# Kernel optimization log

Hardware: AMD Instinct MI355X
Metric: run time of the kernel (lower is better)

The kernel has to match this reference:

```python
import jax, jax.numpy as jnp
import numpy as np

NUM_CLUSTERS = 16
HIDDEN = 1024
BOTTLENECK = 128
N_TOKENS = 65536


def setup_inputs() -> dict:
    key = jax.random.key(0)
    k_h, k_ids, k_w1, k_b1, k_w2, k_b2 = jax.random.split(key, 6)
    h = jax.random.normal(k_h, (N_TOKENS, HIDDEN), dtype=jnp.float32)
    cluster_ids = jax.random.randint(k_ids, (N_TOKENS,), 0, NUM_CLUSTERS)
    # Stacked per-cluster adapter params (torch Linear: y = x @ W.T + b; we store
    # already-transposed weights so forward is x @ W1[c]).
    s1 = 1.0 / np.sqrt(HIDDEN)
    s2 = 1.0 / np.sqrt(BOTTLENECK)
    W1 = jax.random.uniform(k_w1, (NUM_CLUSTERS, HIDDEN, BOTTLENECK), jnp.float32, -s1, s1)
    b1 = jax.random.uniform(k_b1, (NUM_CLUSTERS, BOTTLENECK), jnp.float32, -s1, s1)
    # Original inits these to zero; use small random values so grads are non-trivial.
    W2 = jax.random.uniform(k_w2, (NUM_CLUSTERS, BOTTLENECK, HIDDEN), jnp.float32, -s2, s2) * 0.02
    b2 = jax.random.uniform(k_b2, (NUM_CLUSTERS, HIDDEN), jnp.float32, -s2, s2) * 0.02
    return {"h": h, "cluster_ids": cluster_ids, "W1": W1, "b1": b1, "W2": W2, "b2": b2}


def reference(h, cluster_ids, W1, b1, W2, b2):
    # h: [N, H]; cluster_ids: [N]; W1: [K, H, B]; b1: [K, B]; W2: [K, B, H]; b2: [K, H]
    # out[n] = h[n] + adapter_{cluster_ids[n]}(h[n])
    K = W1.shape[0]
    out = jnp.zeros_like(h)
    for c in range(K):  # fixed small expert count; select per-token result via where
        mid = jax.nn.gelu(h @ W1[c] + b1[c], approximate=False)  # [N, B]
        y = h + mid @ W2[c] + b2[c]                               # [N, H]
        out = jnp.where((cluster_ids == c)[:, None], y, out)
    return out
```

## Files before the change

kernel.cpp:

```cpp
#include <hip/hip_runtime.h>
#include <hip/hip_bf16.h>
#include <math.h>

#define NUM_CLUSTERS 16
#define HIDDEN 1024
#define BOT 128
#define NTOK 65536

typedef __attribute__((ext_vector_type(8))) short bf16x8;
typedef __attribute__((ext_vector_type(4))) float f32x4;

typedef __attribute__((address_space(3))) unsigned int lds_u32;
typedef const __attribute__((address_space(1))) unsigned int glb_u32;

__device__ __forceinline__ void gload16(const void* g, void* l) {
  __builtin_amdgcn_global_load_lds((glb_u32*)g, (lds_u32*)l, 16, 0, 0);
}

__device__ __forceinline__ unsigned short f2bf(float x) {
  union { float f; unsigned u; } v; v.f = x;
  unsigned r = v.u + 0x7fffu + ((v.u >> 16) & 1u);
  return (unsigned short)(r >> 16);
}

__device__ __forceinline__ bf16x8 pack8(float4 a, float4 b) {
  bf16x8 r;
  r[0] = (short)f2bf(a.x); r[1] = (short)f2bf(a.y);
  r[2] = (short)f2bf(a.z); r[3] = (short)f2bf(a.w);
  r[4] = (short)f2bf(b.x); r[5] = (short)f2bf(b.y);
  r[6] = (short)f2bf(b.z); r[7] = (short)f2bf(b.w);
  return r;
}

#define SWZS(row, sidx) ((sidx) ^ (((row) & 7) << 3))
#define SW4(row, fidx) ((fidx) ^ (((row) & 7) << 2))

__device__ __forceinline__ int xcd_swz(int bid, int nwg) {
  const int nx = 8;
  int q = nwg / nx, r = nwg % nx;
  int xcd = bid % nx, idx = bid / nx;
  int b = (xcd < r) ? xcd * (q + 1) : r * (q + 1) + (xcd - r) * q;
  return b + idx;
}


__global__ void k_zero(int* p) {
  if (threadIdx.x < 64) p[threadIdx.x] = 0;
}

__global__ void k_hist(const int* __restrict__ ids, int* __restrict__ counts) {
  __shared__ int lh[NUM_CLUSTERS];
  if (threadIdx.x < NUM_CLUSTERS) lh[threadIdx.x] = 0;
  __syncthreads();
  int i = blockIdx.x * blockDim.x + threadIdx.x;
  int stride = gridDim.x * blockDim.x;
  for (; i < NTOK; i += stride) atomicAdd(&lh[ids[i]], 1);
  __syncthreads();
  if (threadIdx.x < NUM_CLUSTERS) atomicAdd(&counts[threadIdx.x], lh[threadIdx.x]);
}

__global__ void k_scan(const int* __restrict__ counts, int* __restrict__ offsets,
                       int* __restrict__ cursor) {
  if (threadIdx.x == 0 && blockIdx.x == 0) {
    int s = 0;
    for (int c = 0; c < NUM_CLUSTERS; ++c) {
      offsets[c] = s; cursor[c] = s; s += counts[c];
    }
    offsets[NUM_CLUSTERS] = s;
  }
}

__global__ void k_scatter(const int* __restrict__ ids, int* cursor,
                          int* __restrict__ perm) {
  __shared__ int lh[NUM_CLUSTERS], lbase[NUM_CLUSTERS];
  const int tid = threadIdx.x;
  if (tid < NUM_CLUSTERS) lh[tid] = 0;
  __syncthreads();
  const int i = blockIdx.x * 256 + tid;
  const int cc = ids[i];
  const int r = atomicAdd(&lh[cc], 1);
  __syncthreads();
  if (tid < NUM_CLUSTERS) lbase[tid] = atomicAdd(&cursor[tid], lh[tid]);
  __syncthreads();
  perm[lbase[cc] + r] = i;
}

__global__ void k_w1til(const float* __restrict__ W1, unsigned short* __restrict__ outw) {
  const int id = blockIdx.x * 256 + threadIdx.x;
  const int c  = id >> 14;
  const int ks = (id >> 10) & 15;
  const int q  = id & 1023;
  const int o  = q << 4;
  const int row = o >> 7;
  const int lb  = (o & 127) ^ ((row & 7) << 4);
  const int k0  = ks * 64 + (lb >> 1);
  const float* src = W1 + ((size_t)c * HIDDEN + k0) * BOT + row;
  unsigned short v[8];
  #pragma unroll
  for (int j = 0; j < 8; ++j) v[j] = f2bf(src[(size_t)j * BOT]);
  *(uint4*)((char*)outw + ((size_t)(c * 16 + ks)) * 16384 + o) = *(const uint4*)v;
}

__global__ void k_w2til(const float* __restrict__ W2, unsigned short* __restrict__ outw) {
  const int id = blockIdx.x * 256 + threadIdx.x;
  const int c  = id >> 14;
  const int nc = (id >> 10) & 15;
  const int q  = id & 1023;
  const int o  = q << 4;
  const int row = o >> 8;
  const int lb  = (o & 255) ^ ((row & 7) << 4);
  const int b0  = lb >> 1;
  const int n   = nc * 64 + row;
  const float* src = W2 + ((size_t)c * BOT + b0) * HIDDEN + n;
  unsigned short v[8];
  #pragma unroll
  for (int j = 0; j < 8; ++j) v[j] = f2bf(src[(size_t)j * HIDDEN]);
  *(uint4*)((char*)outw + ((size_t)(c * 16 + nc)) * 16384 + o) = *(const uint4*)v;
}

__device__ __forceinline__ bool locate(const int* offsets, int bid, int TMv,
                                       int& c, int& base, int& nvalid) {
  int t = bid;
  for (c = 0; c < NUM_CLUSTERS; ++c) {
    int cnt = offsets[c + 1] - offsets[c];
    int nt = (cnt + TMv - 1) / TMv;
    if (t < nt) {
      base = offsets[c] + t * TMv;
      nvalid = min(TMv, offsets[c + 1] - base);
      return true;
    }
    t -= nt;
  }
  return false;
}

#define SA1 72

__global__ __launch_bounds__(256, 3) void k_gemm1(
    const float* __restrict__ h, const float* __restrict__ b1g,
    const unsigned short* __restrict__ W1til, const int* __restrict__ offsets,
    const int* __restrict__ perm, unsigned short* __restrict__ midg) {

  __shared__ __align__(16) unsigned short sA[2][64 * SA1];
  __shared__ __align__(16) unsigned short sB[2][8192];
  __shared__ int sTok[64];

  const int tid = threadIdx.x;
  const int l = tid & 63, w = tid >> 6;
  const int lr = l & 15, lg = l >> 4;
  const int wr = w >> 1, wc = w & 1;

  const int nwg = NTOK / 64 + NUM_CLUSTERS;
  int c, base, nvalid;
  if (!locate(offsets, xcd_swz(blockIdx.x, nwg), 64, c, base, nvalid)) return;

  if (tid < 64) sTok[tid] = perm[base + min(tid, nvalid - 1)];
  __syncthreads();

  const unsigned short* w1base = W1til + (size_t)c * 16 * 8192;
  const int row = tid >> 2, q4 = tid & 3;
  const float* hrow = h + (long)sTok[row] * HIDDEN + q4 * 16;

  float4 va[4];
  #pragma unroll
  for (int j = 0; j < 4; ++j) va[j] = *(const float4*)(hrow + j * 4);
  #pragma unroll
  for (int j = 0; j < 4; ++j)
    gload16(w1base + j * 2048 + tid * 8, &sB[0][j * 2048 + tid * 8]);
  *(bf16x8*)&sA[0][row * SA1 + q4 * 16]     = pack8(va[0], va[1]);
  *(bf16x8*)&sA[0][row * SA1 + q4 * 16 + 8] = pack8(va[2], va[3]);
  __syncthreads();

  f32x4 acc[2][4];
  #pragma unroll
  for (int i = 0; i < 2; ++i)
    #pragma unroll
    for (int j = 0; j < 4; ++j) { f32x4 z = {0.f, 0.f, 0.f, 0.f}; acc[i][j] = z; }

  for (int t = 0; t < 16; ++t) {
    const int cur = t & 1;
    if (t < 15) {
      #pragma unroll
      for (int j = 0; j < 4; ++j) va[j] = *(const float4*)(hrow + (t + 1) * 64 + j * 4);
      #pragma unroll
      for (int j = 0; j < 4; ++j)
        gload16(w1base + (t + 1) * 8192 + j * 2048 + tid * 8,
                &sB[cur ^ 1][j * 2048 + tid * 8]);
    }
    #pragma unroll
    for (int kk = 0; kk < 2; ++kk) {
      bf16x8 af[2], bfr[4];
      #pragma unroll
      for (int mf = 0; mf < 2; ++mf) {
        const int m = wr * 32 + mf * 16 + lr;
        af[mf] = *(const bf16x8*)&sA[cur][m * SA1 + kk * 32 + lg * 8];
      }
      #pragma unroll
      for (int nf = 0; nf < 4; ++nf) {
        const int rn = wc * 64 + nf * 16 + lr;
        bfr[nf] = *(const bf16x8*)&sB[cur][SWZS(rn, rn * 64 + kk * 32 + lg * 8)];
      }
      #pragma unroll
      for (int mf = 0; mf < 2; ++mf)
        #pragma unroll
        for (int nf = 0; nf < 4; ++nf)
          acc[mf][nf] = __builtin_amdgcn_mfma_f32_16x16x32_bf16(af[mf], bfr[nf], acc[mf][nf], 0, 0, 0);
    }
    if (t < 15) {
      *(bf16x8*)&sA[cur ^ 1][row * SA1 + q4 * 16]     = pack8(va[0], va[1]);
      *(bf16x8*)&sA[cur ^ 1][row * SA1 + q4 * 16 + 8] = pack8(va[2], va[3]);
    }
    __syncthreads();
  }

  float b1v[4];
  #pragma unroll
  for (int nf = 0; nf < 4; ++nf) b1v[nf] = b1g[c * BOT + wc * 64 + nf * 16 + lr];
  #pragma unroll
  for (int mf = 0; mf < 2; ++mf) {
    #pragma unroll
    for (int nf = 0; nf < 4; ++nf) {
      #pragma unroll
      for (int r = 0; r < 4; ++r) {
        float x = acc[mf][nf][r] + b1v[nf];
        float g = 0.5f * x * (1.0f + erff(x * 0.70710678118654752f));
        const int m = wr * 32 + mf * 16 + lg * 4 + r;
        if (m < nvalid) {
          const int n = wc * 64 + nf * 16 + lr;
          midg[(size_t)(base + m) * BOT + n] = f2bf(g);
        }
      }
    }
  }
}


__global__ __launch_bounds__(512, 6) void k_gemm2(
    const float* __restrict__ h, const float* __restrict__ b2g,
    const unsigned short* __restrict__ W2til, const int* __restrict__ offsets,
    const int* __restrict__ perm, const unsigned short* __restrict__ midg,
    float* __restrict__ out) {

  __shared__ __align__(16) unsigned short sM[8192];
  __shared__ __align__(16) unsigned short sB[2][8192];
  __shared__ int sTok[64];

  const int tid = threadIdx.x;
  const int l = tid & 63, w = tid >> 6;
  const int lr = l & 15, lg = l >> 4;
  const int wr = w >> 2, wc = w & 3;

  const int nwg = NTOK / 64 + NUM_CLUSTERS;
  int c, base, nvalid;
  if (!locate(offsets, xcd_swz(blockIdx.x, nwg), 64, c, base, nvalid)) return;

  if (tid < 64) sTok[tid] = perm[base + min(tid, nvalid - 1)];

  const unsigned short* w2base = W2til + (size_t)c * 16 * 8192;

  gload16(w2base + tid * 8, &sB[0][tid * 8]);
  gload16(w2base + 4096 + tid * 8, &sB[0][4096 + tid * 8]);
  {
    const int row = tid >> 3, oct = tid & 7;
    const int srow = base + min(row, nvalid - 1);
    const uint4* ms = (const uint4*)(midg + (size_t)srow * BOT + oct * 16);
    uint4 m0 = ms[0], m1 = ms[1];
    *(uint4*)&sM[SWZS(row, row * 128 + oct * 16)]     = m0;
    *(uint4*)&sM[SWZS(row, row * 128 + oct * 16 + 8)] = m1;
  }
  __syncthreads();

  const int erow = tid >> 3, eo = tid & 7;
  const long etok = (long)sTok[erow] * HIDDEN;
  const float* hrow = h + etok;
  float* orow = out + etok;
  const bool evalid = erow < nvalid;

  for (int nc = 0; nc < 16; ++nc) {
    const int cur = nc & 1;
    if (nc < 15) {
      const unsigned short* w2s = w2base + (nc + 1) * 8192;
      gload16(w2s + tid * 8, &sB[cur ^ 1][tid * 8]);
      gload16(w2s + 4096 + tid * 8, &sB[cur ^ 1][4096 + tid * 8]);
    }
    float4 hv0 = *(const float4*)(hrow + nc * 64 + eo * 8);
    float4 hv1 = *(const float4*)(hrow + nc * 64 + eo * 8 + 4);
    float4 bv0 = *(const float4*)(b2g + c * HIDDEN + nc * 64 + eo * 8);
    float4 bv1 = *(const float4*)(b2g + c * HIDDEN + nc * 64 + eo * 8 + 4);

    f32x4 acc[2];
    { f32x4 z = {0.f, 0.f, 0.f, 0.f}; acc[0] = z; acc[1] = z; }
    #pragma unroll
    for (int kk = 0; kk < 4; ++kk) {
      bf16x8 af[2], bf1;
      #pragma unroll
      for (int mf = 0; mf < 2; ++mf) {
        const int m = wr * 32 + mf * 16 + lr;
        af[mf] = *(const bf16x8*)&sM[SWZS(m, m * 128 + kk * 32 + lg * 8)];
      }
      const int rn = wc * 16 + lr;
      bf1 = *(const bf16x8*)&sB[cur][SWZS(rn, rn * 128 + kk * 32 + lg * 8)];
      #pragma unroll
      for (int mf = 0; mf < 2; ++mf)
        acc[mf] = __builtin_amdgcn_mfma_f32_16x16x32_bf16(af[mf], bf1, acc[mf], 0, 0, 0);
    }
    __syncthreads();

    float* sOutF = (float*)&sB[cur][0];
    #pragma unroll
    for (int mf = 0; mf < 2; ++mf) {
      #pragma unroll
      for (int r = 0; r < 4; ++r) {
        const int m = wr * 32 + mf * 16 + lg * 4 + r;
        const int n = wc * 16 + lr;
        sOutF[SW4(m, m * 64 + n)] = acc[mf][r];
      }
    }
    __syncthreads();

    if (evalid) {
      const int fb = erow * 64 + eo * 8;
      const float4 y0 = *(const float4*)&sOutF[SW4(erow, fb)];
      const float4 y1 = *(const float4*)&sOutF[SW4(erow, fb + 4)];
      float4 o0, o1;
      o0.x = y0.x + hv0.x + bv0.x; o0.y = y0.y + hv0.y + bv0.y;
      o0.z = y0.z + hv0.z + bv0.z; o0.w = y0.w + hv0.w + bv0.w;
      o1.x = y1.x + hv1.x + bv1.x; o1.y = y1.y + hv1.y + bv1.y;
      o1.z = y1.z + hv1.z + bv1.z; o1.w = y1.w + hv1.w + bv1.w;
      *(float4*)(orow + nc * 64 + eo * 8)     = o0;
      *(float4*)(orow + nc * 64 + eo * 8 + 4) = o1;
    }
    __syncthreads();
  }
}

#define FSWZ(row, sidx) ((sidx) ^ (((row) & 7) << 3))

__global__ __launch_bounds__(256, 2) void k_fused(
    const float* __restrict__ h, const float* __restrict__ b1g,
    const float* __restrict__ b2g, const unsigned short* __restrict__ W1til,
    const unsigned short* __restrict__ W2til, const int* __restrict__ offsets,
    const int* __restrict__ perm, float* __restrict__ out) {

  __shared__ __align__(16) unsigned short sAB[16384];
  __shared__ __align__(16) unsigned short sMid[16384];
  __shared__ int sTok[128];

  const int tid = threadIdx.x;
  const int l = tid & 63, w = tid >> 6;
  const int wr = w >> 1, wc = w & 1;
  const int lr = l & 15, lg = l >> 4;

  int c, base, nvalid;
  if (!locate(offsets, blockIdx.x, 128, c, base, nvalid)) return;

  if (tid < 128) sTok[tid] = perm[base + min(tid, nvalid - 1)];
  __syncthreads();

  const unsigned short* w1base = W1til + (size_t)c * 16 * 8192;
  const unsigned short* w2base = W2til + (size_t)c * 16 * 8192;

  const int arow = tid >> 1, ahalf = tid & 1;
  const long htok = (long)sTok[arow] * HIDDEN;

  f32x4 acc[4][4];
  #pragma unroll
  for (int i = 0; i < 4; ++i)
    #pragma unroll
    for (int j = 0; j < 4; ++j) { f32x4 z = {0.f, 0.f, 0.f, 0.f}; acc[i][j] = z; }

  for (int ks = 0; ks < 16; ++ks) {
    __syncthreads();
    const unsigned short* w1s = w1base + ks * 8192;
    #pragma unroll
    for (int j = 0; j < 4; ++j)
      gload16(w1s + j * 2048 + tid * 8, &sAB[8192 + j * 2048 + tid * 8]);
    {
      const float* hp = h + htok + ks * 64 + ahalf * 32;
      float4 v0 = *(const float4*)(hp + 0),  v1 = *(const float4*)(hp + 4);
      float4 v2 = *(const float4*)(hp + 8),  v3 = *(const float4*)(hp + 12);
      float4 v4 = *(const float4*)(hp + 16), v5 = *(const float4*)(hp + 20);
      float4 v6 = *(const float4*)(hp + 24), v7 = *(const float4*)(hp + 28);
      const int sb = arow * 64 + ahalf * 32;
      *(bf16x8*)&sAB[FSWZ(arow, sb + 0)]  = pack8(v0, v1);
      *(bf16x8*)&sAB[FSWZ(arow, sb + 8)]  = pack8(v2, v3);
      *(bf16x8*)&sAB[FSWZ(arow, sb + 16)] = pack8(v4, v5);
      *(bf16x8*)&sAB[FSWZ(arow, sb + 24)] = pack8(v6, v7);
    }
    __syncthreads();
    #pragma unroll
    for (int kk = 0; kk < 2; ++kk) {
      bf16x8 af[4], bfr[4];
      #pragma unroll
      for (int mf = 0; mf < 4; ++mf) {
        const int row = wr * 64 + mf * 16 + lr;
        af[mf] = *(const bf16x8*)&sAB[FSWZ(row, row * 64 + kk * 32 + lg * 8)];
      }
      #pragma unroll
      for (int nf = 0; nf < 4; ++nf) {
        const int rn = wc * 64 + nf * 16 + lr;
        bfr[nf] = *(const bf16x8*)&sAB[8192 + FSWZ(rn, rn * 64 + kk * 32 + lg * 8)];
      }
      #pragma unroll
      for (int mf = 0; mf < 4; ++mf)
        #pragma unroll
        for (int nf = 0; nf < 4; ++nf)
          acc[mf][nf] = __builtin_amdgcn_mfma_f32_16x16x32_bf16(af[mf], bfr[nf], acc[mf][nf], 0, 0, 0);
    }
  }

  float b1v[4];
  #pragma unroll
  for (int nf = 0; nf < 4; ++nf) b1v[nf] = b1g[c * BOT + wc * 64 + nf * 16 + lr];
  #pragma unroll
  for (int mf = 0; mf < 4; ++mf)
    #pragma unroll
    for (int nf = 0; nf < 4; ++nf)
      #pragma unroll
      for (int r = 0; r < 4; ++r) {
        float x = acc[mf][nf][r] + b1v[nf];
        float g = 0.5f * x * (1.0f + erff(x * 0.70710678118654752f));
        const int m = wr * 64 + mf * 16 + lg * 4 + r;
        const int n = wc * 64 + nf * 16 + lr;
        sMid[FSWZ(m, m * 128 + n)] = f2bf(g);
      }

  for (int nc = 0; nc < 16; ++nc) {
    __syncthreads();
    #pragma unroll
    for (int j = 0; j < 4; ++j)
      gload16(w2base + nc * 8192 + j * 2048 + tid * 8, &sAB[j * 2048 + tid * 8]);
    __syncthreads();

    f32x4 a2[4][2];
    #pragma unroll
    for (int i = 0; i < 4; ++i)
      #pragma unroll
      for (int j = 0; j < 2; ++j) { f32x4 z = {0.f, 0.f, 0.f, 0.f}; a2[i][j] = z; }

    #pragma unroll
    for (int kk = 0; kk < 4; ++kk) {
      bf16x8 af[4], bfr[2];
      #pragma unroll
      for (int mf = 0; mf < 4; ++mf) {
        const int m = wr * 64 + mf * 16 + lr;
        af[mf] = *(const bf16x8*)&sMid[FSWZ(m, m * 128 + kk * 32 + lg * 8)];
      }
      #pragma unroll
      for (int nf = 0; nf < 2; ++nf) {
        const int rn = wc * 32 + nf * 16 + lr;
        bfr[nf] = *(const bf16x8*)&sAB[FSWZ(rn, rn * 128 + kk * 32 + lg * 8)];
      }
      #pragma unroll
      for (int mf = 0; mf < 4; ++mf)
        #pragma unroll
        for (int nf = 0; nf < 2; ++nf)
          a2[mf][nf] = __builtin_amdgcn_mfma_f32_16x16x32_bf16(af[mf], bfr[nf], a2[mf][nf], 0, 0, 0);
    }

    #pragma unroll
    for (int nf = 0; nf < 2; ++nf) {
      const int nn = nc * 64 + wc * 32 + nf * 16 + lr;
      const float b2v = b2g[c * HIDDEN + nn];
      #pragma unroll
      for (int mf = 0; mf < 4; ++mf)
        #pragma unroll
        for (int r = 0; r < 4; ++r) {
          const int m = wr * 64 + mf * 16 + lg * 4 + r;
          if (m < nvalid) {
            const long tk = (long)sTok[m] * HIDDEN;
            out[tk + nn] = h[tk + nn] + a2[mf][nf][r] + b2v;
          }
        }
    }
  }
}

extern "C" void kernel_launch(void* const* d_in, const int* in_sizes, int n_in,
                              void* d_out, int out_size, void* d_ws, size_t ws_size,
                              hipStream_t stream) {
  const float* h   = (const float*)d_in[0];
  const int*   ids = (const int*)d_in[1];
  const float* W1  = (const float*)d_in[2];
  const float* b1  = (const float*)d_in[3];
  const float* W2  = (const float*)d_in[4];
  const float* b2  = (const float*)d_in[5];
  float* out = (float*)d_out;

  char* ws = (char*)d_ws;
  int* counts  = (int*)ws;
  int* cursor  = (int*)(ws + 64);
  int* offsets = (int*)(ws + 128);
  int* perm    = (int*)(ws + 256);
  unsigned short* W1til = (unsigned short*)(ws + 262400);
  unsigned short* W2til = W1til + (size_t)16 * 16 * 8192;
  unsigned short* midg  = W2til + (size_t)16 * 16 * 8192;
  const size_t need = 262400 + 2 * (size_t)16 * 16 * 8192 * 2 +
                      (size_t)NTOK * BOT * 2;

  k_zero<<<1, 64, 0, stream>>>(counts);
  k_hist<<<256, 256, 0, stream>>>(ids, counts);
  k_scan<<<1, 64, 0, stream>>>(counts, offsets, cursor);
  k_scatter<<<NTOK / 256, 256, 0, stream>>>(ids, cursor, perm);
  k_w1til<<<1024, 256, 0, stream>>>(W1, W1til);
  k_w2til<<<1024, 256, 0, stream>>>(W2, W2til);

  if (ws_size >= need) {
    const int nwg = NTOK / 64 + NUM_CLUSTERS;
    k_gemm1<<<nwg, 256, 0, stream>>>(h, b1, W1til, offsets, perm, midg);
    k_gemm2<<<nwg, 512, 0, stream>>>(h, b2, W2til, offsets, perm, midg, out);
  } else {
    k_fused<<<NTOK / 128 + NUM_CLUSTERS, 256, 0, stream>>>(
        h, b1, b2, W1til, W2til, offsets, perm, out);
  }
}
```

Baseline: 290.6 us.

## Prefetch activations two stages ahead with manual vmcnt waits in W1 GEMM

The first-layer GEMM loop now loads h rows two K-steps ahead into alternating register buffers. The full __syncthreads is replaced by explicit s_waitcnt vmcnt/lgkmcnt counts plus raw s_barrier, and the loop is fully unrolled. The aim is to keep more global loads in flight and stop the compiler inserting conservative waits on every outstanding load. In exchange it uses more registers, and the hand-tuned wait counts depend on the exact number of memory instructions issued, so they break if that changes.

```diff
diff --git a/kernel.cpp b/kernel.cpp
--- a/kernel.cpp
+++ b/kernel.cpp
@@ -161,15 +161,20 @@
   const int row = tid >> 2, q4 = tid & 3;
   const float* hrow = h + (long)sTok[row] * HIDDEN + q4 * 16;
 
-  float4 va[4];
-  #pragma unroll
-  for (int j = 0; j < 4; ++j) va[j] = *(const float4*)(hrow + j * 4);
+  float4 vaA[4], vaB[4];
+  #pragma unroll
+  for (int j = 0; j < 4; ++j) vaA[j] = *(const float4*)(hrow + j * 4);
   #pragma unroll
   for (int j = 0; j < 4; ++j)
     gload16(w1base + j * 2048 + tid * 8, &sB[0][j * 2048 + tid * 8]);
-  *(bf16x8*)&sA[0][row * SA1 + q4 * 16]     = pack8(va[0], va[1]);
-  *(bf16x8*)&sA[0][row * SA1 + q4 * 16 + 8] = pack8(va[2], va[3]);
-  __syncthreads();
+  #pragma unroll
+  for (int j = 0; j < 4; ++j) vaB[j] = *(const float4*)(hrow + 64 + j * 4);
+  *(bf16x8*)&sA[0][row * SA1 + q4 * 16]     = pack8(vaA[0], vaA[1]);
+  *(bf16x8*)&sA[0][row * SA1 + q4 * 16 + 8] = pack8(vaA[2], vaA[3]);
+  asm volatile("s_waitcnt lgkmcnt(0)" ::: "memory");
+  __builtin_amdgcn_sched_barrier(0);
+  __builtin_amdgcn_s_barrier();
+  __builtin_amdgcn_sched_barrier(0);
 
   f32x4 acc[2][4];
   #pragma unroll
@@ -177,16 +182,31 @@
     #pragma unroll
     for (int j = 0; j < 4; ++j) { f32x4 z = {0.f, 0.f, 0.f, 0.f}; acc[i][j] = z; }
 
+  #pragma unroll
   for (int t = 0; t < 16; ++t) {
     const int cur = t & 1;
     if (t < 15) {
-      #pragma unroll
-      for (int j = 0; j < 4; ++j) va[j] = *(const float4*)(hrow + (t + 1) * 64 + j * 4);
+      const unsigned short* w1s = w1base + (t + 1) * 8192;
       #pragma unroll
       for (int j = 0; j < 4; ++j)
-        gload16(w1base + (t + 1) * 8192 + j * 2048 + tid * 8,
-                &sB[cur ^ 1][j * 2048 + tid * 8]);
-    }
+        gload16(w1s + j * 2048 + tid * 8, &sB[cur ^ 1][j * 2048 + tid * 8]);
+    }
+    if (t < 14) {
+      if (t & 1) {
+        #pragma unroll
+        for (int j = 0; j < 4; ++j) vaB[j] = *(const float4*)(hrow + (t + 2) * 64 + j * 4);
+      } else {
+        #pragma unroll
+        for (int j = 0; j < 4; ++j) vaA[j] = *(const float4*)(hrow + (t + 2) * 64 + j * 4);
+      }
+    }
+    if (t < 14)       asm volatile("s_waitcnt vmcnt(12)" ::: "memory");
+    else if (t == 14) asm volatile("s_waitcnt vmcnt(8)" ::: "memory");
+    else              asm volatile("s_waitcnt vmcnt(0)" ::: "memory");
+    __builtin_amdgcn_sched_barrier(0);
+    __builtin_amdgcn_s_barrier();
+    __builtin_amdgcn_sched_barrier(0);
+
     #pragma unroll
     for (int kk = 0; kk < 2; ++kk) {
       bf16x8 af[2], bfr[4];
@@ -206,11 +226,16 @@
         for (int nf = 0; nf < 4; ++nf)
           acc[mf][nf] = __builtin_amdgcn_mfma_f32_16x16x32_bf16(af[mf], bfr[nf], acc[mf][nf], 0, 0, 0);
     }
+
     if (t < 15) {
-      *(bf16x8*)&sA[cur ^ 1][row * SA1 + q4 * 16]     = pack8(va[0], va[1]);
-      *(bf16x8*)&sA[cur ^ 1][row * SA1 + q4 * 16 + 8] = pack8(va[2], va[3]);
-    }
-    __syncthreads();
+      const float4* src = ((t + 1) & 1) ? vaB : vaA;
+      *(bf16x8*)&sA[cur ^ 1][row * SA1 + q4 * 16]     = pack8(src[0], src[1]);
+      *(bf16x8*)&sA[cur ^ 1][row * SA1 + q4 * 16 + 8] = pack8(src[2], src[3]);
+      asm volatile("s_waitcnt lgkmcnt(0)" ::: "memory");
+      __builtin_amdgcn_sched_barrier(0);
+      __builtin_amdgcn_s_barrier();
+      __builtin_amdgcn_sched_barrier(0);
+    }
   }
 
   float b1v[4];
```

Result: faster. 278.7 us (-4.1%).

## Widen gemm1 to 512 threads and replace syncthreads with explicit vmcnt waits

Applied to the files above, without the earlier changes.

gemm1 now runs 8 waves per block with a 2x4 wave grid and an XOR-swizzled A tile. Its K loop is unrolled in pairs with explicit s_waitcnt vmcnt counts and raw barriers, so the prefetch of the next h and W1 slices overlaps the MFMA work. gemm2 swaps __syncthreads for partial vmcnt waits plus raw barriers and issues the h and bias loads earlier. The hand-counted vmcnt values are fragile: if the compiler emits a different number of memory ops than assumed, the waits can allow races or stall more than needed.

```diff
diff --git a/kernel.cpp b/kernel.cpp
--- a/kernel.cpp
+++ b/kernel.cpp
@@ -34,6 +34,15 @@
 
 #define SWZS(row, sidx) ((sidx) ^ (((row) & 7) << 3))
 #define SW4(row, fidx) ((fidx) ^ (((row) & 7) << 2))
+
+#define VMW(n) asm volatile("s_waitcnt vmcnt(" #n ")" ::: "memory")
+#define SBAR()                                  \
+  do {                                          \
+    __builtin_amdgcn_sched_barrier(0);          \
+    __builtin_amdgcn_s_barrier();               \
+    __builtin_amdgcn_sched_barrier(0);          \
+  } while (0)
+#define LGKM0() asm volatile("s_waitcnt lgkmcnt(0)" ::: "memory")
 
 __device__ __forceinline__ int xcd_swz(int bid, int nwg) {
   const int nx = 8;
@@ -134,21 +143,20 @@
   return false;
 }
 
-#define SA1 72
-
-__global__ __launch_bounds__(256, 3) void k_gemm1(
+
+__global__ __launch_bounds__(512, 6) void k_gemm1(
     const float* __restrict__ h, const float* __restrict__ b1g,
     const unsigned short* __restrict__ W1til, const int* __restrict__ offsets,
     const int* __restrict__ perm, unsigned short* __restrict__ midg) {
 
-  __shared__ __align__(16) unsigned short sA[2][64 * SA1];
+  __shared__ __align__(16) unsigned short sA[2][4096];
   __shared__ __align__(16) unsigned short sB[2][8192];
   __shared__ int sTok[64];
 
   const int tid = threadIdx.x;
   const int l = tid & 63, w = tid >> 6;
   const int lr = l & 15, lg = l >> 4;
-  const int wr = w >> 1, wc = w & 1;
+  const int wr = w >> 2, wc = w & 3;
 
   const int nwg = NTOK / 64 + NUM_CLUSTERS;
   int c, base, nvalid;
@@ -158,75 +166,101 @@
   __syncthreads();
 
   const unsigned short* w1base = W1til + (size_t)c * 16 * 8192;
-  const int row = tid >> 2, q4 = tid & 3;
-  const float* hrow = h + (long)sTok[row] * HIDDEN + q4 * 16;
-
-  float4 va[4];
-  #pragma unroll
-  for (int j = 0; j < 4; ++j) va[j] = *(const float4*)(hrow + j * 4);
-  #pragma unroll
-  for (int j = 0; j < 4; ++j)
-    gload16(w1base + j * 2048 + tid * 8, &sB[0][j * 2048 + tid * 8]);
-  *(bf16x8*)&sA[0][row * SA1 + q4 * 16]     = pack8(va[0], va[1]);
-  *(bf16x8*)&sA[0][row * SA1 + q4 * 16 + 8] = pack8(va[2], va[3]);
-  __syncthreads();
-
-  f32x4 acc[2][4];
+  const int row = tid >> 3, o8 = tid & 7;
+  const float* hrow = h + (long)sTok[row] * HIDDEN + o8 * 8;
+
+  float4 vaA[2], vaB[2];
+  vaA[0] = *(const float4*)(hrow);       vaA[1] = *(const float4*)(hrow + 4);
+  gload16(w1base + tid * 8, &sB[0][tid * 8]);
+  gload16(w1base + 4096 + tid * 8, &sB[0][4096 + tid * 8]);
+  vaB[0] = *(const float4*)(hrow + 64);  vaB[1] = *(const float4*)(hrow + 68);
+  *(bf16x8*)&sA[0][SWZS(row, row * 64 + o8 * 8)] = pack8(vaA[0], vaA[1]);
+  LGKM0();
+  SBAR();
+
+  f32x4 acc[2][2];
   #pragma unroll
   for (int i = 0; i < 2; ++i)
     #pragma unroll
-    for (int j = 0; j < 4; ++j) { f32x4 z = {0.f, 0.f, 0.f, 0.f}; acc[i][j] = z; }
-
-  for (int t = 0; t < 16; ++t) {
-    const int cur = t & 1;
-    if (t < 15) {
-      #pragma unroll
-      for (int j = 0; j < 4; ++j) va[j] = *(const float4*)(hrow + (t + 1) * 64 + j * 4);
-      #pragma unroll
-      for (int j = 0; j < 4; ++j)
-        gload16(w1base + (t + 1) * 8192 + j * 2048 + tid * 8,
-                &sB[cur ^ 1][j * 2048 + tid * 8]);
-    }
-    #pragma unroll
-    for (int kk = 0; kk < 2; ++kk) {
-      bf16x8 af[2], bfr[4];
-      #pragma unroll
-      for (int mf = 0; mf < 2; ++mf) {
-        const int m = wr * 32 + mf * 16 + lr;
-        af[mf] = *(const bf16x8*)&sA[cur][m * SA1 + kk * 32 + lg * 8];
-      }
-      #pragma unroll
-      for (int nf = 0; nf < 4; ++nf) {
-        const int rn = wc * 64 + nf * 16 + lr;
-        bfr[nf] = *(const bf16x8*)&sB[cur][SWZS(rn, rn * 64 + kk * 32 + lg * 8)];
-      }
-      #pragma unroll
-      for (int mf = 0; mf < 2; ++mf)
-        #pragma unroll
-        for (int nf = 0; nf < 4; ++nf)
-          acc[mf][nf] = __builtin_amdgcn_mfma_f32_16x16x32_bf16(af[mf], bfr[nf], acc[mf][nf], 0, 0, 0);
-    }
-    if (t < 15) {
-      *(bf16x8*)&sA[cur ^ 1][row * SA1 + q4 * 16]     = pack8(va[0], va[1]);
-      *(bf16x8*)&sA[cur ^ 1][row * SA1 + q4 * 16 + 8] = pack8(va[2], va[3]);
-    }
-    __syncthreads();
-  }
-
-  float b1v[4];
-  #pragma unroll
-  for (int nf = 0; nf < 4; ++nf) b1v[nf] = b1g[c * BOT + wc * 64 + nf * 16 + lr];
+    for (int j = 0; j < 2; ++j) { f32x4 z = {0.f, 0.f, 0.f, 0.f}; acc[i][j] = z; }
+
+#define G1_MFMA(CUR)                                                          \
+  do {                                                                        \
+    _Pragma("unroll")                                                         \
+    for (int kk = 0; kk < 2; ++kk) {                                          \
+      bf16x8 af[2], bfr[2];                                                   \
+      _Pragma("unroll")                                                       \
+      for (int mf = 0; mf < 2; ++mf) {                                        \
+        const int m = wr * 32 + mf * 16 + lr;                                 \
+        af[mf] = *(const bf16x8*)&sA[CUR][SWZS(m, m * 64 + kk * 32 + lg * 8)];\
+      }                                                                       \
+      _Pragma("unroll")                                                       \
+      for (int nf = 0; nf < 2; ++nf) {                                        \
+        const int rn = wc * 32 + nf * 16 + lr;                                \
+        bfr[nf] = *(const bf16x8*)&sB[CUR][SWZS(rn, rn * 64 + kk * 32 + lg * 8)]; \
+      }                                                                       \
+      _Pragma("unroll")                                                       \
+      for (int mf = 0; mf < 2; ++mf)                                          \
+        _Pragma("unroll")                                                     \
+        for (int nf = 0; nf < 2; ++nf)                                        \
+          acc[mf][nf] = __builtin_amdgcn_mfma_f32_16x16x32_bf16(              \
+              af[mf], bfr[nf], acc[mf][nf], 0, 0, 0);                         \
+    }                                                                         \
+  } while (0)
+
+#define G1_ISSUE_B(T, NXT)                                                    \
+  do {                                                                        \
+    const unsigned short* w1s = w1base + (T + 1) * 8192;                      \
+    gload16(w1s + tid * 8, &sB[NXT][tid * 8]);                                \
+    gload16(w1s + 4096 + tid * 8, &sB[NXT][4096 + tid * 8]);                  \
+  } while (0)
+
+#define G1_STAGE(SRC, NXT)                                                    \
+  do {                                                                        \
+    *(bf16x8*)&sA[NXT][SWZS(row, row * 64 + o8 * 8)] = pack8(SRC[0], SRC[1]); \
+    LGKM0();                                                                  \
+    SBAR();                                                                   \
+  } while (0)
+
+  for (int tp = 0; tp < 14; tp += 2) {
+    G1_ISSUE_B(tp, 1);
+    vaA[0] = *(const float4*)(hrow + (tp + 2) * 64);
+    vaA[1] = *(const float4*)(hrow + (tp + 2) * 64 + 4);
+    VMW(6);
+    SBAR();
+    G1_MFMA(0);
+    G1_STAGE(vaB, 1);
+    G1_ISSUE_B(tp + 1, 0);
+    vaB[0] = *(const float4*)(hrow + (tp + 3) * 64);
+    vaB[1] = *(const float4*)(hrow + (tp + 3) * 64 + 4);
+    VMW(6);
+    SBAR();
+    G1_MFMA(1);
+    G1_STAGE(vaA, 0);
+  }
+  G1_ISSUE_B(14, 1);
+  VMW(4);
+  SBAR();
+  G1_MFMA(0);
+  G1_STAGE(vaB, 1);
+  VMW(0);
+  SBAR();
+  G1_MFMA(1);
+
+  float b1v[2];
+  #pragma unroll
+  for (int nf = 0; nf < 2; ++nf) b1v[nf] = b1g[c * BOT + wc * 32 + nf * 16 + lr];
   #pragma unroll
   for (int mf = 0; mf < 2; ++mf) {
     #pragma unroll
-    for (int nf = 0; nf < 4; ++nf) {
+    for (int nf = 0; nf < 2; ++nf) {
       #pragma unroll
       for (int r = 0; r < 4; ++r) {
         float x = acc[mf][nf][r] + b1v[nf];
         float g = 0.5f * x * (1.0f + erff(x * 0.70710678118654752f));
         const int m = wr * 32 + mf * 16 + lg * 4 + r;
         if (m < nvalid) {
-          const int n = wc * 64 + nf * 16 + lr;
+          const int n = wc * 32 + nf * 16 + lr;
           midg[(size_t)(base + m) * BOT + n] = f2bf(g);
         }
       }
@@ -258,17 +292,18 @@
 
   const unsigned short* w2base = W2til + (size_t)c * 16 * 8192;
 
-  gload16(w2base + tid * 8, &sB[0][tid * 8]);
-  gload16(w2base + 4096 + tid * 8, &sB[0][4096 + tid * 8]);
   {
     const int row = tid >> 3, oct = tid & 7;
     const int srow = base + min(row, nvalid - 1);
     const uint4* ms = (const uint4*)(midg + (size_t)srow * BOT + oct * 16);
     uint4 m0 = ms[0], m1 = ms[1];
+    gload16(w2base + tid * 8, &sB[0][tid * 8]);
+    gload16(w2base + 4096 + tid * 8, &sB[0][4096 + tid * 8]);
     *(uint4*)&sM[SWZS(row, row * 128 + oct * 16)]     = m0;
     *(uint4*)&sM[SWZS(row, row * 128 + oct * 16 + 8)] = m1;
   }
-  __syncthreads();
+  LGKM0();
+  SBAR();
 
   const int erow = tid >> 3, eo = tid & 7;
   const long etok = (long)sTok[erow] * HIDDEN;
@@ -278,15 +313,17 @@
 
   for (int nc = 0; nc < 16; ++nc) {
     const int cur = nc & 1;
+    float4 hv0 = *(const float4*)(hrow + nc * 64 + eo * 8);
+    float4 hv1 = *(const float4*)(hrow + nc * 64 + eo * 8 + 4);
+    float4 bv0 = *(const float4*)(b2g + c * HIDDEN + nc * 64 + eo * 8);
+    float4 bv1 = *(const float4*)(b2g + c * HIDDEN + nc * 64 + eo * 8 + 4);
     if (nc < 15) {
       const unsigned short* w2s = w2base + (nc + 1) * 8192;
       gload16(w2s + tid * 8, &sB[cur ^ 1][tid * 8]);
       gload16(w2s + 4096 + tid * 8, &sB[cur ^ 1][4096 + tid * 8]);
     }
-    float4 hv0 = *(const float4*)(hrow + nc * 64 + eo * 8);
-    float4 hv1 = *(const float4*)(hrow + nc * 64 + eo * 8 + 4);
-    float4 bv0 = *(const float4*)(b2g + c * HIDDEN + nc * 64 + eo * 8);
-    float4 bv1 = *(const float4*)(b2g + c * HIDDEN + nc * 64 + eo * 8 + 4);
+    if (nc == 0 || nc == 15) { VMW(6); } else { VMW(8); }
+    SBAR();
 
     f32x4 acc[2];
     { f32x4 z = {0.f, 0.f, 0.f, 0.f}; acc[0] = z; acc[1] = z; }
@@ -304,7 +341,7 @@
       for (int mf = 0; mf < 2; ++mf)
         acc[mf] = __builtin_amdgcn_mfma_f32_16x16x32_bf16(af[mf], bf1, acc[mf], 0, 0, 0);
     }
-    __syncthreads();
+    SBAR();
 
     float* sOutF = (float*)&sB[cur][0];
     #pragma unroll
@@ -316,7 +353,8 @@
         sOutF[SW4(m, m * 64 + n)] = acc[mf][r];
       }
     }
-    __syncthreads();
+    LGKM0();
+    SBAR();
 
     if (evalid) {
       const int fb = erow * 64 + eo * 8;
@@ -330,7 +368,7 @@
       *(float4*)(orow + nc * 64 + eo * 8)     = o0;
       *(float4*)(orow + nc * 64 + eo * 8 + 4) = o1;
     }
-    __syncthreads();
+    SBAR();
   }
 }
 
@@ -507,7 +545,7 @@
 
   if (ws_size >= need) {
     const int nwg = NTOK / 64 + NUM_CLUSTERS;
-    k_gemm1<<<nwg, 256, 0, stream>>>(h, b1, W1til, offsets, perm, midg);
+    k_gemm1<<<nwg, 512, 0, stream>>>(h, b1, W1til, offsets, perm, midg);
     k_gemm2<<<nwg, 512, 0, stream>>>(h, b2, W2til, offsets, perm, midg, out);
   } else {
     k_fused<<<NTOK / 128 + NUM_CLUSTERS, 256, 0, stream>>>(
```

Result: faster. 269.9 us (-7.1%).
